# Optimization experiments

Measured on AMD Instinct MI355X. Metric: run time of the kernel, lower is better.

Reference implementation:

```python
import jax, jax.numpy as jnp
import numpy as np

B, S, D = 1, 4096, 1024
H, KVH, HD = 16, 4, 64  # heads, kv heads, head_dim; GQA groups = H//KVH
EOS_PROB = 0.05


def rotate_half(x):
    h = x.shape[-1] // 2
    return jnp.concatenate([-x[..., h:], x[..., :h]], axis=-1)


def setup_inputs() -> dict:
    key = jax.random.key(0)
    ks = jax.random.split(key, 8)
    hidden_states = jax.random.normal(ks[0], (B, S, D), jnp.float32) * 0.02
    # standard RoPE tables, [B, S, HD]
    inv_freq = 1.0 / (10000.0 ** (jnp.arange(0, HD, 2, dtype=jnp.float32) / HD))
    freqs = jnp.outer(jnp.arange(S, dtype=jnp.float32), inv_freq)
    emb = jnp.concatenate([freqs, freqs], axis=-1)
    cos = jnp.broadcast_to(jnp.cos(emb)[None], (B, S, HD))
    sin = jnp.broadcast_to(jnp.sin(emb)[None], (B, S, HD))
    sc = D ** -0.5
    Wq = jax.random.normal(ks[1], (D, H * HD), jnp.float32) * sc
    Wk = jax.random.normal(ks[2], (D, KVH * HD), jnp.float32) * sc
    Wv = jax.random.normal(ks[3], (D, KVH * HD), jnp.float32) * sc
    Wo = jax.random.normal(ks[4], (H * HD, D), jnp.float32) * sc
    # sentence-boundary (end-of-sentence / special) token mask, ~1 EOS per 20 tokens
    special = (jax.random.uniform(ks[5], (B, S)) < EOS_PROB).astype(jnp.int32)
    special = special.at[:, 0].set(1)  # BOS acts as a boundary token
    # closest end-of-sentence token index at or before each position
    pos = jnp.arange(S, dtype=jnp.int32)
    marked = jnp.where(special.astype(bool), pos[None, :], jnp.int32(-1))
    eos_idx = jax.lax.associative_scan(jnp.maximum, marked, axis=1)
    eos_idx = jnp.maximum(eos_idx, 0).astype(jnp.int32)
    return {
        'hidden_states': hidden_states, 'cos': cos, 'sin': sin,
        'Wq': Wq, 'Wk': Wk, 'Wv': Wv, 'Wo': Wo,
        'special_embeddings_mask': special,
        'clothest_end_of_sentence_token_idx': eos_idx,
    }


def reference(hidden_states, cos, sin, Wq, Wk, Wv, Wo,
              special_embeddings_mask, clothest_end_of_sentence_token_idx):
    b, s, d = hidden_states.shape
    # projections -> [b, h, s, hd]
    q = (hidden_states @ Wq).reshape(b, s, H, HD).transpose(0, 2, 1, 3)
    k = (hidden_states @ Wk).reshape(b, s, KVH, HD).transpose(0, 2, 1, 3)
    v = (hidden_states @ Wv).reshape(b, s, KVH, HD).transpose(0, 2, 1, 3)
    # RoPE
    c = cos[:, None, :, :]
    sn = sin[:, None, :, :]
    q = q * c + rotate_half(q) * sn
    k = k * c + rotate_half(k) * sn
    # GQA: repeat kv heads
    groups = H // KVH
    k = jnp.repeat(k, groups, axis=1)
    v = jnp.repeat(v, groups, axis=1)
    scores = jnp.einsum('bhqd,bhkd->bhqk', q, k) * (HD ** -0.5)
    # sentence-structured mask: causal AND (key inside current sentence OR key is
    # an end-of-sentence/special boundary token)
    pos = jnp.arange(s, dtype=jnp.int32)
    causal = (pos[None, :] <= pos[:, None])[None, None]           # [1,1,s,s]
    special_k = special_embeddings_mask.astype(bool)[:, None, None, :]  # [b,1,1,s]
    eos = clothest_end_of_sentence_token_idx[:, None, :, None]    # [b,1,s,1]
    allowed = causal & ((pos[None, None, None, :] >= eos) | special_k)
    scores = jnp.where(allowed, scores, jnp.asarray(-1e9, scores.dtype))
    probs = jax.nn.softmax(scores, axis=-1)
    attn = jnp.einsum('bhqk,bhkd->bhqd', probs, v)
    attn = attn.transpose(0, 2, 1, 3).reshape(b, s, H * HD)
    return attn @ Wo
```

## Files before the change

### kernel.cpp

```cpp
#include <hip/hip_runtime.h>

typedef __bf16 bf16x8 __attribute__((ext_vector_type(8)));
typedef float f32x4 __attribute__((ext_vector_type(4)));
typedef short s16x8 __attribute__((ext_vector_type(8)));
typedef short s16x4 __attribute__((ext_vector_type(4)));
typedef unsigned short u16;
typedef unsigned int u32;
typedef unsigned long long u64;

#define S_LEN 4096
#define DMODEL 1024
#define NH 16
#define HD 64

static __device__ __forceinline__ u16 f2bf(float f) {
  union { float f; u32 u; } a; a.f = f;
  u32 r = (a.u + 0x7fffu + ((a.u >> 16) & 1u)) >> 16;
  return (u16)r;
}

static __device__ __forceinline__ f32x4 mfma16(bf16x8 a, bf16x8 b, f32x4 c) {
  return __builtin_amdgcn_mfma_f32_16x16x32_bf16(a, b, c, 0, 0, 0);
}

static __device__ __forceinline__ f32x4 mfma16x16(s16x4 a, s16x4 b, f32x4 c) {
#if __has_builtin(__builtin_amdgcn_mfma_f32_16x16x16bf16_1k)
  return __builtin_amdgcn_mfma_f32_16x16x16bf16_1k(a, b, c, 0, 0, 0);
#else
  asm("v_mfma_f32_16x16x16_bf16 %0, %1, %2, %0" : "+v"(c) : "v"(a), "v"(b));
  return c;
#endif
}

static __device__ __forceinline__ void gload16(const void* g, void* l) {
  __builtin_amdgcn_global_load_lds((const __attribute__((address_space(1))) u32*)g,
                                   (__attribute__((address_space(3))) u32*)l, 16, 0, 0);
}

#define WAIT_VM(N) asm volatile("s_waitcnt vmcnt(" #N ")" ::: "memory")
static __device__ __forceinline__ void sbar() { __builtin_amdgcn_s_barrier(); }
static __device__ __forceinline__ void spin() { __builtin_amdgcn_sched_barrier(0); }

static __device__ __forceinline__ int xcd_swz(int id, int nwg) {
  return (id & 7) * (nwg >> 3) + (id >> 3);
}

__global__ __launch_bounds__(256)
void prep_kernel(const float* __restrict__ hidden, const float* __restrict__ Wq,
                 const float* __restrict__ Wk, const float* __restrict__ Wv,
                 const float* __restrict__ Wo, const int* __restrict__ spec,
                 const int* __restrict__ eosi,
                 u16* __restrict__ hbf, u16* __restrict__ wqkvT, u16* __restrict__ woT,
                 u64* __restrict__ spb, int* __restrict__ sidx, int* __restrict__ scnt,
                 int4* __restrict__ qmeta) {
  __shared__ float ftile[32][33];
  __shared__ u64 smask[64];
  __shared__ int scnt_s[64];
  __shared__ int spref[64];

  const int bx = (int)blockIdx.x;
  const int t = (int)threadIdx.x;

  if (bx < 4096) {
    const int i = (bx * 256 + t) * 4;
    const float4 v = *(const float4*)(hidden + i);
    uint2 o;
    o.x = (u32)f2bf(v.x) | ((u32)f2bf(v.y) << 16);
    o.y = (u32)f2bf(v.z) | ((u32)f2bf(v.w) << 16);
    *(uint2*)(hbf + i) = o;
    return;
  }
  if (bx < 6656) {
    const float* W; u16* WT; int N, loc, nbx;
    if (bx < 5120)      { W = Wq; WT = wqkvT;               N = 1024; loc = bx - 4096; nbx = 32; }
    else if (bx < 5376) { W = Wk; WT = wqkvT + 1024 * 1024; N = 256;  loc = bx - 5120; nbx = 8; }
    else if (bx < 5632) { W = Wv; WT = wqkvT + 1280 * 1024; N = 256;  loc = bx - 5376; nbx = 8; }
    else                { W = Wo; WT = woT;                 N = 1024; loc = bx - 5632; nbx = 32; }
    const int n0 = (loc % nbx) * 32, k0 = (loc / nbx) * 32;
    const int tx = t & 31, ty = t >> 5;
#pragma unroll
    for (int i = 0; i < 4; ++i)
      ftile[ty + 8 * i][tx] = W[(size_t)(k0 + ty + 8 * i) * N + n0 + tx];
    __syncthreads();
#pragma unroll
    for (int i = 0; i < 4; ++i)
      WT[(size_t)(n0 + ty + 8 * i) * 1024 + k0 + tx] = f2bf(ftile[tx][ty + 8 * i]);
    return;
  }
  const int wv = t >> 6, l = t & 63;
#pragma unroll
  for (int i = 0; i < 16; ++i) {
    const int b = wv * 16 + i;
    const u64 m = __ballot(spec[b * 64 + l] != 0);
    if (l == 0) { smask[b] = m; scnt_s[b] = __popcll(m); }
  }
  __syncthreads();
  if (wv == 0) {
    const int v = scnt_s[l];
    int inc = v;
#pragma unroll
    for (int d = 1; d < 64; d <<= 1) {
      const int o = __shfl_up(inc, d);
      if (l >= d) inc += o;
    }
    spref[l] = inc - v;
    if (l == 63) scnt[0] = inc;
    spb[l] = smask[l];
  }
  __syncthreads();
#pragma unroll
  for (int i = 0; i < 16; ++i) {
    const int b = wv * 16 + i;
    const u64 m = smask[b];
    if ((m >> l) & 1ull)
      sidx[spref[b] + __popcll(m & ((1ull << l) - 1ull))] = b * 64 + l;
  }
  if (t < 64) {
    const int e = eosi[t * 64];
    const int tlo = e >> 6;
    const int nsp = spref[tlo];
    const int nspt = (nsp + 63) >> 6;
    qmeta[t] = make_int4(tlo, nspt, nspt + (t - tlo + 1), nsp);
  }
}

__global__ __launch_bounds__(256)
void pack_kernel(const u16* __restrict__ Kb, const u16* __restrict__ Vtg,
                 const int* __restrict__ sidx, const int* __restrict__ scnt,
                 u16* __restrict__ Kg, u16* __restrict__ Vgt) {
  __shared__ int rowidx[64];
  const int nspec = scnt[0];
  const int j0 = (int)blockIdx.x * 64;
  if (j0 >= nspec) return;
  const int kvh = (int)blockIdx.y;
  const int t = (int)threadIdx.x;
  if (t < 64) rowidx[t] = (j0 + t < nspec) ? sidx[j0 + t] : 0;
  __syncthreads();
  {
    const int r = t >> 2;
    const int s = rowidx[r];
    const int j = j0 + r;
    const u16* srcrow = Kb + (size_t)s * 256 + kvh * 64;
    u16* dstrow = Kg + (size_t)j * 256 + kvh * 64;
    const int x = (j ^ s) & 7;
#pragma unroll
    for (int a = 0; a < 2; ++a) {
      const int cd = (t & 3) * 2 + a;
      *(s16x8*)(dstrow + cd * 8) = *(const s16x8*)(srcrow + ((cd ^ x) * 8));
    }
  }
  {
    const int d = t >> 2;
    const u16* srcrow = Vtg + (size_t)(kvh * 64 + d) * 4096;
    u16* drow = Vgt + (size_t)(kvh * 64 + d) * 4096 + j0;
    const int xd = (d & 7) << 3;
#pragma unroll
    for (int a = 0; a < 2; ++a) {
      const int jc = (t & 3) * 2 + a;
      s16x8 o;
#pragma unroll
      for (int e = 0; e < 8; ++e) {
        const int s = rowidx[jc * 8 + e];
        o[e] = (short)srcrow[(s & ~63) + ((s & 63) ^ xd)];
      }
      *(s16x8*)(drow + ((jc * 8) ^ xd)) = o;
    }
  }
}

template <int MODE>
__global__ __launch_bounds__(256, 3)
void gemm128(const u16* __restrict__ A, const u16* __restrict__ BT,
             const float* __restrict__ cosp, const float* __restrict__ sinp,
             u16* __restrict__ Qb, u16* __restrict__ Kb, u16* __restrict__ Vtg,
             float* __restrict__ Cf) {
  __shared__ __align__(16) u16 As[2][128 * 64];
  __shared__ __align__(16) u16 Bs[2][64 * 64];
  const int t = (int)threadIdx.x;
  const int w = t >> 6;
  const int lane = t & 63;
  const int lr = lane & 15, lg = lane >> 4;

  const int nx = (int)gridDim.x;
  const int nwg = nx * (int)gridDim.y;
  const int id = xcd_swz((int)blockIdx.x + (int)blockIdx.y * nx, nwg);
  const int m0 = (id / nx) * 128;
  const int n0 = (id % nx) * 64;
  const int wm = w * 32;

  f32x4 acc[2][4] = {};

  const int srow = t >> 3;
  const int sp = t & 7;

  auto STAGE = [&](int buf, int k0) {
#pragma unroll
    for (int i = 0; i < 4; ++i) {
      const int j = i * 32 + srow;
      gload16(A + (size_t)(m0 + j) * 1024 + k0 + ((sp ^ (j & 7)) * 8),
              &As[buf][i * 2048 + t * 8]);
    }
#pragma unroll
    for (int i = 0; i < 2; ++i) {
      const int j = i * 32 + srow;
      gload16(BT + (size_t)(n0 + j) * 1024 + k0 + ((sp ^ (j & 7)) * 8),
              &Bs[buf][i * 2048 + t * 8]);
    }
  };

  STAGE(0, 0);

  for (int it = 0; it < 16; ++it) {
    const int cur = it & 1;
    if (it < 15) {
      STAGE(cur ^ 1, (it + 1) * 64);
      WAIT_VM(6);
    } else {
      WAIT_VM(0);
    }
    spin();
    sbar();
#pragma unroll
    for (int c = 0; c < 2; ++c) {
      bf16x8 af[2], bg[4];
#pragma unroll
      for (int mi = 0; mi < 2; ++mi) {
        const int row = wm + mi * 16 + lr;
        af[mi] = *(const bf16x8*)&As[cur][row * 64 + (((c * 4 + lg) ^ (row & 7)) * 8)];
      }
#pragma unroll
      for (int ni = 0; ni < 4; ++ni) {
        const int row = ni * 16 + lr;
        bg[ni] = *(const bf16x8*)&Bs[cur][row * 64 + (((c * 4 + lg) ^ (row & 7)) * 8)];
      }
#pragma unroll
      for (int mi = 0; mi < 2; ++mi)
#pragma unroll
        for (int ni = 0; ni < 4; ++ni)
          acc[mi][ni] = mfma16(af[mi], bg[ni], acc[mi][ni]);
    }
    spin();
    sbar();
  }

  if (MODE == 0) {
#pragma unroll
    for (int mi = 0; mi < 2; ++mi)
#pragma unroll
      for (int r = 0; r < 4; ++r) {
        const int m = m0 + wm + mi * 16 + lg * 4 + r;
#pragma unroll
        for (int ni = 0; ni < 4; ++ni)
          Cf[(size_t)m * 1024 + n0 + ni * 16 + lr] = acc[mi][ni][r];
      }
  } else if (n0 < 1280) {
#pragma unroll
    for (int mi = 0; mi < 2; ++mi)
#pragma unroll
      for (int r = 0; r < 4; ++r) {
        const int m = m0 + wm + mi * 16 + lg * 4 + r;
        const float* cr = cosp + (size_t)m * 64;
        const float* sr = sinp + (size_t)m * 64;
        float o[4];
#pragma unroll
        for (int ni = 0; ni < 2; ++ni) {
          const int d1 = ni * 16 + lr, d2 = d1 + 32;
          const float x = acc[mi][ni][r], y = acc[mi][ni + 2][r];
          o[ni]     = x * cr[d1] - y * sr[d1];
          o[ni + 2] = y * cr[d2] + x * sr[d2];
        }
        if (n0 < 1024) {
          u16* dst = Qb + (size_t)m * 1024 + n0;
#pragma unroll
          for (int ni = 0; ni < 4; ++ni) dst[ni * 16 + lr] = f2bf(o[ni]);
        } else {
          u16* dst = Kb + (size_t)m * 256 + (n0 - 1024);
          const int sw = (m & 7) << 3;
#pragma unroll
          for (int ni = 0; ni < 4; ++ni) dst[(ni * 16 + lr) ^ sw] = f2bf(o[ni]);
        }
      }
  } else {
    const int kvh = (n0 - 1280) >> 6;
#pragma unroll
    for (int ni = 0; ni < 4; ++ni) {
      const int d = ni * 16 + lr;
      u16* vrow = Vtg + (size_t)(kvh * 64 + d) * 4096;
      const int xd = (d & 7) << 3;
#pragma unroll
      for (int mi = 0; mi < 2; ++mi) {
        const int sb = m0 + wm + mi * 16 + lg * 4;
        const int os = (sb & ~63) | ((sb & 63) ^ xd);
        uint2 pkv;
        pkv.x = (u32)f2bf(acc[mi][ni][0]) | ((u32)f2bf(acc[mi][ni][1]) << 16);
        pkv.y = (u32)f2bf(acc[mi][ni][2]) | ((u32)f2bf(acc[mi][ni][3]) << 16);
        *(uint2*)(vrow + os) = pkv;
      }
    }
  }
}

__global__ __launch_bounds__(256, 5)
void attn_kernel(const u16* __restrict__ Qb, const u16* __restrict__ Kb,
                 const u16* __restrict__ Vtg, const u16* __restrict__ Kg,
                 const u16* __restrict__ Vgt, const u64* __restrict__ spb,
                 const int* __restrict__ eosi, const int4* __restrict__ qmeta,
                 u16* __restrict__ Ob) {
  __shared__ __align__(16) u16 lds[2][2][4096];

  const int id = xcd_swz((int)blockIdx.x + (int)blockIdx.y * 64, 1024);
  const int qt = 63 - (id & 63);
  const int h = id >> 6;
  const int kvh = h >> 2;
  const int t = (int)threadIdx.x;
  const int w = t >> 6;
  const int lane = t & 63;
  const int lr = lane & 15, lg = lane >> 4;
  const int q0 = qt * 64;
  const int q = q0 + w * 16 + lr;
  const int swl = (lr & 7) << 3;

  const int4 qm = qmeta[qt];
  const int tile_lo = qm.x;
  const int nit = qm.z;
  const int nsp = qm.w;
  const int nloc = qt - tile_lo + 1;

  bf16x8 aq[2];
  {
    const u16* qp = Qb + (size_t)q * 1024 + h * 64 + lg * 8;
    aq[0] = *(const bf16x8*)qp;
    aq[1] = *(const bf16x8*)(qp + 32);
  }
  const int eos_q = eosi[q];

  f32x4 acc[4] = {};
  float mrow = -3.0e38f;
  float lrow = 0.0f;

  const int grow = t >> 3;
  const int gcol = (t & 7) * 8;

  auto STAGE = [&](int buf, int it) {
    const u16 *kp, *vp;
    if (it < nloc) {
      const int kbase = (tile_lo + it) * 64;
      kp = Kb + (size_t)kbase * 256 + kvh * 64;
      vp = Vtg + (size_t)(kvh * 64) * 4096 + kbase;
    } else {
      const int jb = (it - nloc) * 64;
      kp = Kg + (size_t)jb * 256 + kvh * 64;
      vp = Vgt + (size_t)(kvh * 64) * 4096 + jb;
    }
#pragma unroll
    for (int i = 0; i < 2; ++i) {
      gload16(kp + (size_t)(i * 32 + grow) * 256 + gcol, &lds[buf][0][i * 2048 + t * 8]);
      gload16(vp + (size_t)(i * 32 + grow) * 4096 + gcol, &lds[buf][1][i * 2048 + t * 8]);
    }
  };

  STAGE(0, 0);

  for (int it = 0; it < nit; ++it) {
    if (it + 1 < nit) {
      STAGE((it + 1) & 1, it + 1);
      WAIT_VM(4);
    } else {
      WAIT_VM(0);
    }
    spin();
    sbar();
    const u16* Kl = &lds[it & 1][0][0];
    const u16* Vl = &lds[it & 1][1][0];

    f32x4 st[4];
#pragma unroll
    for (int kt = 0; kt < 4; ++kt) {
      f32x4 s = {};
#pragma unroll
      for (int c = 0; c < 2; ++c) {
        bf16x8 ak = *(const bf16x8*)(Kl + (kt * 16 + lr) * 64 + ((c * 32 + lg * 8) ^ swl));
        s = mfma16(ak, aq[c], s);
      }
      st[kt] = s;
    }

    u64 allowed;
    if (it < nloc) {
      const int kbase = (tile_lo + it) * 64;
      const u64 spec = spb[tile_lo + it];
      const int dq = q - kbase;
      const u64 causal = (dq >= 63) ? ~0ull : ((2ull << dq) - 1ull);
      const int de = eos_q - kbase;
      const u64 ge = (de <= 0) ? ~0ull : (de >= 64 ? 0ull : (~0ull << de));
      allowed = causal & (ge | spec);
    } else {
      const int rem = nsp - (it - nloc) * 64;
      allowed = (rem >= 64) ? ~0ull : ((1ull << rem) - 1ull);
    }

    float xs[16];
    float tmax = -3.0e38f;
#pragma unroll
    for (int kt = 0; kt < 4; ++kt) {
      const u32 bits = (u32)(allowed >> (kt * 16 + lg * 4)) & 0xFu;
#pragma unroll
      for (int r = 0; r < 4; ++r) {
        const float x = ((bits >> r) & 1u) ? st[kt][r] * 0.18033688011112042f : -3.0e38f;
        xs[kt * 4 + r] = x;
        tmax = fmaxf(tmax, x);
      }
    }
    tmax = fmaxf(tmax, __shfl_xor(tmax, 16));
    tmax = fmaxf(tmax, __shfl_xor(tmax, 32));
    const float mn = fmaxf(mrow, tmax);
    const float resc = exp2f(mrow - mn);
    mrow = mn;

    float rs = 0.0f;
    u32 pk[8];
#pragma unroll
    for (int i = 0; i < 16; i += 2) {
      const float p0 = exp2f(xs[i] - mn);
      const float p1 = exp2f(xs[i + 1] - mn);
      rs += p0 + p1;
      pk[i >> 1] = (u32)f2bf(p0) | ((u32)f2bf(p1) << 16);
    }
    rs += __shfl_xor(rs, 16);
    rs += __shfl_xor(rs, 32);
    lrow = lrow * resc + rs;

#pragma unroll
    for (int dt = 0; dt < 4; ++dt)
#pragma unroll
      for (int r = 0; r < 4; ++r) acc[dt][r] *= resc;

#pragma unroll
    for (int kt = 0; kt < 4; ++kt) {
      union { u32 u[2]; s16x4 v; } cv;
      cv.u[0] = pk[kt * 2]; cv.u[1] = pk[kt * 2 + 1];
      const int vo = (kt * 16 + lg * 4) ^ swl;
#pragma unroll
      for (int dt = 0; dt < 4; ++dt) {
        s16x4 av = *(const s16x4*)(Vl + (dt * 16 + lr) * 64 + vo);
        acc[dt] = mfma16x16(av, cv.v, acc[dt]);
      }
    }
    spin();
    sbar();
  }

  const float inv = 1.0f / lrow;
#pragma unroll
  for (int dt = 0; dt < 4; ++dt) {
    const u32 w0 = (u32)f2bf(acc[dt][0] * inv) | ((u32)f2bf(acc[dt][1] * inv) << 16);
    const u32 w1 = (u32)f2bf(acc[dt][2] * inv) | ((u32)f2bf(acc[dt][3] * inv) << 16);
    u32* dst = (u32*)(Ob + (size_t)q * 1024 + h * 64 + dt * 16 + lg * 4);
    dst[0] = w0; dst[1] = w1;
  }
}

extern "C" void kernel_launch(void* const* d_in, const int* in_sizes, int n_in,
                              void* d_out, int out_size, void* d_ws, size_t ws_size,
                              hipStream_t stream) {
  (void)in_sizes; (void)n_in; (void)out_size; (void)ws_size;
  const float* hidden = (const float*)d_in[0];
  const float* cosp   = (const float*)d_in[1];
  const float* sinp   = (const float*)d_in[2];
  const float* Wq     = (const float*)d_in[3];
  const float* Wk     = (const float*)d_in[4];
  const float* Wv     = (const float*)d_in[5];
  const float* Wo     = (const float*)d_in[6];
  const int* spec     = (const int*)d_in[7];
  const int* eosi     = (const int*)d_in[8];
  float* out = (float*)d_out;

  u16* ws = (u16*)d_ws;
  u16* hbf   = ws;
  u16* wqkvT = hbf + 4194304;
  u16* woT   = wqkvT + 1572864;
  u16* Qb    = woT + 1048576;
  u16* Kb    = Qb + 4194304;
  u16* Vtg   = Kb + 1048576;
  u16* Ob    = Vtg + 1048576;
  u16* tail  = Ob + 4194304;
  u64* spb   = (u64*)tail;
  int* sidx  = (int*)(tail + 256);
  int* scnt  = (int*)(tail + 8448);
  int4* qmeta = (int4*)(tail + 8512);
  u16* Kg    = hbf;
  u16* Vgt   = hbf + 1048576;

  prep_kernel<<<dim3(6657), dim3(256), 0, stream>>>(hidden, Wq, Wk, Wv, Wo, spec, eosi,
                                                    hbf, wqkvT, woT, spb, sidx, scnt, qmeta);
  gemm128<1><<<dim3(24, 32), dim3(256), 0, stream>>>(hbf, wqkvT, cosp, sinp,
                                                     Qb, Kb, Vtg, nullptr);
  pack_kernel<<<dim3(64, 4), dim3(256), 0, stream>>>(Kb, Vtg, sidx, scnt, Kg, Vgt);
  attn_kernel<<<dim3(64, 16), dim3(256), 0, stream>>>(Qb, Kb, Vtg, Kg, Vgt, spb,
                                                      eosi, qmeta, Ob);
  gemm128<0><<<dim3(16, 32), dim3(256), 0, stream>>>(Ob, woT, nullptr, nullptr,
                                                     nullptr, nullptr, nullptr, out);
}
```

Measured before the change: 79.52 us.

## Fuse special-token K/V gather into QKV GEMM epilogue, drop pack kernel

The separate pack kernel that gathered special-token K and V rows into compact buffers is removed. Prep now writes a per-position rank (or -1), and the QKV GEMM epilogue scatters each special row's bf16 K and V values directly into the compact Kg/Vgt buffers. This saves one kernel launch and a re-read of K/V, at the cost of extra rank loads and scattered scalar stores in the GEMM epilogue. Kg/Vgt move to a dedicated workspace region because hbf is still being read during the GEMM.

After: 75.30 us. -5.3%, faster.

```diff
diff --git a/kernel.cpp b/kernel.cpp
--- a/kernel.cpp
+++ b/kernel.cpp
@@ -51,8 +51,7 @@
                  const float* __restrict__ Wo, const int* __restrict__ spec,
                  const int* __restrict__ eosi,
                  u16* __restrict__ hbf, u16* __restrict__ wqkvT, u16* __restrict__ woT,
-                 u64* __restrict__ spb, int* __restrict__ sidx, int* __restrict__ scnt,
-                 int4* __restrict__ qmeta) {
+                 u64* __restrict__ spb, int* __restrict__ srank, int4* __restrict__ qmeta) {
   __shared__ float ftile[32][33];
   __shared__ u64 smask[64];
   __shared__ int scnt_s[64];
@@ -104,7 +103,6 @@
       if (l >= d) inc += o;
     }
     spref[l] = inc - v;
-    if (l == 63) scnt[0] = inc;
     spb[l] = smask[l];
   }
   __syncthreads();
@@ -112,8 +110,8 @@
   for (int i = 0; i < 16; ++i) {
     const int b = wv * 16 + i;
     const u64 m = smask[b];
-    if ((m >> l) & 1ull)
-      sidx[spref[b] + __popcll(m & ((1ull << l) - 1ull))] = b * 64 + l;
+    srank[b * 64 + l] = ((m >> l) & 1ull)
+        ? spref[b] + __popcll(m & ((1ull << l) - 1ull)) : -1;
   }
   if (t < 64) {
     const int e = eosi[t * 64];
@@ -124,55 +122,13 @@
   }
 }
 
-__global__ __launch_bounds__(256)
-void pack_kernel(const u16* __restrict__ Kb, const u16* __restrict__ Vtg,
-                 const int* __restrict__ sidx, const int* __restrict__ scnt,
-                 u16* __restrict__ Kg, u16* __restrict__ Vgt) {
-  __shared__ int rowidx[64];
-  const int nspec = scnt[0];
-  const int j0 = (int)blockIdx.x * 64;
-  if (j0 >= nspec) return;
-  const int kvh = (int)blockIdx.y;
-  const int t = (int)threadIdx.x;
-  if (t < 64) rowidx[t] = (j0 + t < nspec) ? sidx[j0 + t] : 0;
-  __syncthreads();
-  {
-    const int r = t >> 2;
-    const int s = rowidx[r];
-    const int j = j0 + r;
-    const u16* srcrow = Kb + (size_t)s * 256 + kvh * 64;
-    u16* dstrow = Kg + (size_t)j * 256 + kvh * 64;
-    const int x = (j ^ s) & 7;
-#pragma unroll
-    for (int a = 0; a < 2; ++a) {
-      const int cd = (t & 3) * 2 + a;
-      *(s16x8*)(dstrow + cd * 8) = *(const s16x8*)(srcrow + ((cd ^ x) * 8));
-    }
-  }
-  {
-    const int d = t >> 2;
-    const u16* srcrow = Vtg + (size_t)(kvh * 64 + d) * 4096;
-    u16* drow = Vgt + (size_t)(kvh * 64 + d) * 4096 + j0;
-    const int xd = (d & 7) << 3;
-#pragma unroll
-    for (int a = 0; a < 2; ++a) {
-      const int jc = (t & 3) * 2 + a;
-      s16x8 o;
-#pragma unroll
-      for (int e = 0; e < 8; ++e) {
-        const int s = rowidx[jc * 8 + e];
-        o[e] = (short)srcrow[(s & ~63) + ((s & 63) ^ xd)];
-      }
-      *(s16x8*)(drow + ((jc * 8) ^ xd)) = o;
-    }
-  }
-}
-
 template <int MODE>
 __global__ __launch_bounds__(256, 3)
 void gemm128(const u16* __restrict__ A, const u16* __restrict__ BT,
              const float* __restrict__ cosp, const float* __restrict__ sinp,
+             const int* __restrict__ srank,
              u16* __restrict__ Qb, u16* __restrict__ Kb, u16* __restrict__ Vtg,
+             u16* __restrict__ Kg, u16* __restrict__ Vgt,
              float* __restrict__ Cf) {
   __shared__ __align__(16) u16 As[2][128 * 64];
   __shared__ __align__(16) u16 Bs[2][64 * 64];
@@ -274,27 +230,52 @@
 #pragma unroll
           for (int ni = 0; ni < 4; ++ni) dst[ni * 16 + lr] = f2bf(o[ni]);
         } else {
+          u16 hv[4];
+#pragma unroll
+          for (int ni = 0; ni < 4; ++ni) hv[ni] = f2bf(o[ni]);
           u16* dst = Kb + (size_t)m * 256 + (n0 - 1024);
           const int sw = (m & 7) << 3;
 #pragma unroll
-          for (int ni = 0; ni < 4; ++ni) dst[(ni * 16 + lr) ^ sw] = f2bf(o[ni]);
+          for (int ni = 0; ni < 4; ++ni) dst[(ni * 16 + lr) ^ sw] = hv[ni];
+          const int rk = srank[m];
+          if (rk >= 0) {
+            u16* dg = Kg + (size_t)rk * 256 + (n0 - 1024);
+            const int swg = (rk & 7) << 3;
+#pragma unroll
+            for (int ni = 0; ni < 4; ++ni) dg[(ni * 16 + lr) ^ swg] = hv[ni];
+          }
         }
       }
   } else {
     const int kvh = (n0 - 1280) >> 6;
+    int rks[2][4];
+#pragma unroll
+    for (int mi = 0; mi < 2; ++mi)
+#pragma unroll
+      for (int r = 0; r < 4; ++r)
+        rks[mi][r] = srank[m0 + wm + mi * 16 + lg * 4 + r];
 #pragma unroll
     for (int ni = 0; ni < 4; ++ni) {
       const int d = ni * 16 + lr;
       u16* vrow = Vtg + (size_t)(kvh * 64 + d) * 4096;
+      u16* grow_ = Vgt + (size_t)(kvh * 64 + d) * 4096;
       const int xd = (d & 7) << 3;
 #pragma unroll
       for (int mi = 0; mi < 2; ++mi) {
         const int sb = m0 + wm + mi * 16 + lg * 4;
         const int os = (sb & ~63) | ((sb & 63) ^ xd);
+        u16 bv[4];
+#pragma unroll
+        for (int r = 0; r < 4; ++r) bv[r] = f2bf(acc[mi][ni][r]);
         uint2 pkv;
-        pkv.x = (u32)f2bf(acc[mi][ni][0]) | ((u32)f2bf(acc[mi][ni][1]) << 16);
-        pkv.y = (u32)f2bf(acc[mi][ni][2]) | ((u32)f2bf(acc[mi][ni][3]) << 16);
+        pkv.x = (u32)bv[0] | ((u32)bv[1] << 16);
+        pkv.y = (u32)bv[2] | ((u32)bv[3] << 16);
         *(uint2*)(vrow + os) = pkv;
+#pragma unroll
+        for (int r = 0; r < 4; ++r) {
+          const int j = rks[mi][r];
+          if (j >= 0) grow_[(j & ~63) + ((j & 63) ^ xd)] = bv[r];
+        }
       }
     }
   }
@@ -485,19 +466,18 @@
   u16* Ob    = Vtg + 1048576;
   u16* tail  = Ob + 4194304;
   u64* spb   = (u64*)tail;
-  int* sidx  = (int*)(tail + 256);
-  int* scnt  = (int*)(tail + 8448);
-  int4* qmeta = (int4*)(tail + 8512);
-  u16* Kg    = hbf;
-  u16* Vgt   = hbf + 1048576;
+  int* srank = (int*)(tail + 256);
+  int4* qmeta = (int4*)(tail + 8448);
+  u16* Kg    = tail + 8960;
+  u16* Vgt   = Kg + 1048576;
 
   prep_kernel<<<dim3(6657), dim3(256), 0, stream>>>(hidden, Wq, Wk, Wv, Wo, spec, eosi,
-                                                    hbf, wqkvT, woT, spb, sidx, scnt, qmeta);
-  gemm128<1><<<dim3(24, 32), dim3(256), 0, stream>>>(hbf, wqkvT, cosp, sinp,
-                                                     Qb, Kb, Vtg, nullptr);
-  pack_kernel<<<dim3(64, 4), dim3(256), 0, stream>>>(Kb, Vtg, sidx, scnt, Kg, Vgt);
+                                                    hbf, wqkvT, woT, spb, srank, qmeta);
+  gemm128<1><<<dim3(24, 32), dim3(256), 0, stream>>>(hbf, wqkvT, cosp, sinp, srank,
+                                                     Qb, Kb, Vtg, Kg, Vgt, nullptr);
   attn_kernel<<<dim3(64, 16), dim3(256), 0, stream>>>(Qb, Kb, Vtg, Kg, Vgt, spb,
                                                       eosi, qmeta, Ob);
-  gemm128<0><<<dim3(16, 32), dim3(256), 0, stream>>>(Ob, woT, nullptr, nullptr,
-                                                     nullptr, nullptr, nullptr, out);
-}
+  gemm128<0><<<dim3(16, 32), dim3(256), 0, stream>>>(Ob, woT, nullptr, nullptr, nullptr,
+                                                     nullptr, nullptr, nullptr, nullptr,
+                                                     nullptr, out);
+}
```
